# Performance work log

Measured on AMD Instinct MI355X. Metric: run time of the kernel, lower is better.

The kernel has to match this reference:

```python
import jax, jax.numpy as jnp
import numpy as np

N = 4096      # atoms
K = 5         # atoms gathered per cell (top_k in put_atoms_in_cells)
M = 8         # neighbors kept per atom
NBR = 26      # neighbor cells per cell (9+9+8)

def _grid():
    # get_cells: box [-10,10) step 1 Angstrom -> 20^3 = 8000 cells
    g = jnp.arange(-10.0, 10.0, 1.0)
    X = jnp.stack(jnp.meshgrid(g, g, g))       # (3,20,20,20), tf.meshgrid default 'xy'
    return jnp.transpose(X).reshape(-1, 3)      # (8000,3)

def _sqdist(a, b):
    # ||a_i - b_j||^2 via expansion; avoids (A,B,3) intermediate
    return (jnp.sum(a * a, 1)[:, None] + jnp.sum(b * b, 1)[None, :] - 2.0 * (a @ b.T))

def _neighbor_list(coords):
    cells = _grid()                              # (n_cells, 3)
    # put_atoms_in_cells: tf.nn.top_k(norm, k) -> k LARGEST norms (faithful to source)
    d_ca = _sqdist(cells, coords)                # (n_cells, N)
    _, atoms_in_cells = jax.lax.top_k(d_ca, K)   # (n_cells, K)
    # get_cells_for_atoms: top_k(-norm, 1) -> closest cell per atom
    d_ac = _sqdist(coords, cells)                # (N, n_cells)
    cells_for_atoms = jnp.argmin(d_ac, axis=1)   # (N,)
    # compute_neighbor_cells: top_k(norm, 26) (faithful to source)
    d_cc = _sqdist(cells, cells)                 # (n_cells, n_cells)
    _, nbr_cells = jax.lax.top_k(d_cc, NBR)      # (n_cells, 26)
    nbr_cells_atom = nbr_cells[cells_for_atoms]  # (N, 26)
    nbr_inds = atoms_in_cells[nbr_cells_atom]    # (N, 26, K)
    nbr_coords = coords[nbr_inds]                # (N, 26, K, 3)
    dists = jnp.sum((coords[:, None, None, :] - nbr_coords) ** 2, axis=-1)
    dists = dists.reshape(N, NBR * K)            # (N, 130)
    _, locs = jax.lax.top_k(dists, M)            # top_k(dists, M) as in source
    flat = nbr_inds.reshape(N, NBR * K)
    return jnp.take_along_axis(flat, locs, axis=1)   # (N, M) atom indices

def _energy(coords, vdw, weights, nrot, nbr):
    # d_ij = r_ij - R_i - R_j
    diff = coords[:, None, :] - coords[nbr]      # (N, M, 3)
    r = jnp.sqrt(jnp.sum(diff * diff, axis=-1) + 1e-12)
    d = r - vdw[:, None] - vdw[nbr]
    g1 = jnp.exp(-(d / 0.5) ** 2)
    g2 = jnp.exp(-((d - 3.0) / 2.0) ** 2)
    rep = jnp.where(d < 0.0, d * d, 0.0)
    hyd = jnp.where(d < 0.5, 1.0, jnp.where(d < 1.5, 1.5 - d, 0.0))
    hb = jnp.where(d < -0.7, 1.0, jnp.where(d < 0.0, -d / 0.7, 0.0))
    hval = (weights[0] * g1 + weights[1] * g2 + weights[2] * rep
            + weights[3] * hyd + weights[4] * hb)
    f = jnp.where(d < 8.0, hval, 0.0)            # cutoff at 8 Angstrom
    c = jnp.sum(f)
    return c / (1.0 + weights[5] * nrot[0])      # g(c, Nrot)

def setup_inputs() -> dict:
    key = jax.random.key(0)
    k1, k2, k3 = jax.random.split(key, 3)
    coords = jax.random.uniform(k1, (N, 3), jnp.float32, -10.0, 10.0)
    vdw = jax.random.uniform(k2, (N,), jnp.float32, 1.0, 2.0)
    weights = 0.3 * jax.random.normal(k3, (6,), jnp.float32)
    nrot = 8.0 * jnp.ones((1,), jnp.float32)
    return {"coords": coords, "vdw": vdw, "weights": weights, "nrot": nrot}

def reference(coords, vdw, weights, nrot):
    nbr = _neighbor_list(coords)
    return _energy(coords, vdw, weights, nrot, nbr)
```

## Files before the change

kernel.cpp:

```cpp
#include <hip/hip_runtime.h>
#include <stdint.h>

#define NATOMS 4096
#define NCELLS 8000
#define KTOP 5
#define MNBR 8
#define NBRC 26
#define HBINS 184
#define LSTMAX 512

__device__ __forceinline__ unsigned long long umax64(unsigned long long a, unsigned long long b) {
    return a > b ? a : b;
}
__device__ __forceinline__ unsigned long long umin64(unsigned long long a, unsigned long long b) {
    return a < b ? a : b;
}

__device__ __forceinline__ void cell_coords_i(int m, int& x, int& y, int& z) {
    int a = m / 400;
    int r = m - a * 400;
    int b = r / 20;
    int c = r - b * 20;
    x = b - 10; y = c - 10; z = a - 10;
}

__global__ __launch_bounds__(256) void k1_cells_nbr(const float* __restrict__ coords,
                                                    int* __restrict__ cellsForAtoms,
                                                    float* __restrict__ sumsq,
                                                    int* __restrict__ nbrTable,
                                                    int* __restrict__ neededFlag) {
    const int atom = blockIdx.x;
    const int t = threadIdx.x;
    const int lane = t & 63;

    __shared__ int sCi;
    __shared__ uint32_t h[HBINS];
    __shared__ int lst[LSTMAX];
    __shared__ int sV, cnt;

    if (t < HBINS) h[t] = 0;
    if (t == 0) cnt = 0;

    if (t < 64) {
        float ax = coords[atom * 3], ay = coords[atom * 3 + 1], az = coords[atom * 3 + 2];
        float sa = __fadd_rn(__fadd_rn(__fmul_rn(ax, ax), __fmul_rn(ay, ay)), __fmul_rn(az, az));

        int fx = (int)floorf(ax), fy = (int)floorf(ay), fz = (int)floorf(az);
        int vx = min(9, max(-10, fx - 1 + (lane & 3)));
        int vy = min(9, max(-10, fy - 1 + ((lane >> 2) & 3)));
        int vz = min(9, max(-10, fz - 1 + (lane >> 4)));
        int m = (vz + 10) * 400 + (vx + 10) * 20 + (vy + 10);

        float cx = (float)vx, cy = (float)vy, cz = (float)vz;
        float scell = (float)(vx * vx + vy * vy + vz * vz);
        float dot = __fadd_rn(__fadd_rn(__fmul_rn(ax, cx), __fmul_rn(ay, cy)), __fmul_rn(az, cz));
        float val = __fsub_rn(__fadd_rn(sa, scell), __fmul_rn(2.0f, dot));
        unsigned long long key = ((unsigned long long)__float_as_uint(val) << 32) | (unsigned int)m;

        for (int off = 32; off > 0; off >>= 1)
            key = umin64(key, (unsigned long long)__shfl_xor((long long)key, off));
        if (lane == 0) {
            int c = (int)(key & 0xFFFFFFFFull);
            cellsForAtoms[atom] = c;
            sumsq[atom] = sa;
            sCi = c;
        }
    }
    __syncthreads();

    const int ci = sCi;
    int xi, yi, zi;
    cell_coords_i(ci, xi, yi, zi);
    const int Lx = max(xi + 10, 9 - xi);
    const int Ly = max(yi + 10, 9 - yi);
    const int Lz = max(zi + 10, 9 - zi);
    const int lo = (Lx - 2) * (Lx - 2) + (Ly - 2) * (Ly - 2) + (Lz - 2) * (Lz - 2)
                 + 2 * min(Lx, min(Ly, Lz)) - 3;
    const int A0 = zi + 10;

#pragma unroll
    for (int col = 0; col < 2; ++col) {
        int p = t + 256 * col;
        if (p < 400) {
            int bb = p / 20, cc = p - bb * 20;
            int dxv = xi - (bb - 10), dyv = yi - (cc - 10);
            int Dbc = dxv * dxv + dyv * dyv;
            int a = 0;
            for (; a < 20; ++a) {
                int dz = A0 - a;
                int d = Dbc + dz * dz;
                if (d < lo) break;
                atomicAdd(&h[d - lo], 1u);
            }
            if (a < 20) {
                for (int a2 = 19; a2 >= a; --a2) {
                    int dz = A0 - a2;
                    int d = Dbc + dz * dz;
                    if (d < lo) break;
                    atomicAdd(&h[d - lo], 1u);
                }
            }
        }
    }
    __syncthreads();

    if (t < 64) {
        int c4[4];
        int cnt4 = 0;
#pragma unroll
        for (int k = 0; k < 4; ++k) {
            int b = (HBINS - 1) - (t * 4 + k);
            c4[k] = (b >= 0) ? (int)h[b] : 0;
            cnt4 += c4[k];
        }
        int incl = cnt4;
        for (int off = 1; off < 64; off <<= 1) {
            int v = __shfl_up(incl, off);
            if (lane >= off) incl += v;
        }
        int P = incl - cnt4;
        if (P < NBRC && incl >= NBRC) {
            int run = P;
#pragma unroll
            for (int k = 0; k < 4; ++k) {
                run += c4[k];
                if (run >= NBRC) { sV = lo + (HBINS - 1) - (t * 4 + k); break; }
            }
        }
    }
    __syncthreads();
    const int V = sV;

#pragma unroll
    for (int col = 0; col < 2; ++col) {
        int p = t + 256 * col;
        if (p < 400) {
            int bb = p / 20, cc = p - bb * 20;
            int dxv = xi - (bb - 10), dyv = yi - (cc - 10);
            int Dbc = dxv * dxv + dyv * dyv;
            int a = 0;
            for (; a < 20; ++a) {
                int dz = A0 - a;
                int d = Dbc + dz * dz;
                if (d < V) break;
                int q = atomicAdd(&cnt, 1);
                if (q < LSTMAX) lst[q] = (d << 13) | (8191 - (a * 400 + p));
            }
            if (a < 20) {
                for (int a2 = 19; a2 >= a; --a2) {
                    int dz = A0 - a2;
                    int d = Dbc + dz * dz;
                    if (d < V) break;
                    int q = atomicAdd(&cnt, 1);
                    if (q < LSTMAX) lst[q] = (d << 13) | (8191 - (a2 * 400 + p));
                }
            }
        }
    }
    __syncthreads();

    int n = min(cnt, LSTMAX);
    for (int idx = t; idx < n; idx += 256) {
        int key = lst[idx];
        int rank = 0;
        for (int m = 0; m < n; ++m) rank += (lst[m] > key) ? 1 : 0;
        if (rank < NBRC) {
            int j = 8191 - (key & 8191);
            nbrTable[ci * NBRC + rank] = j;
            neededFlag[j] = 1;
        }
    }
}

__global__ __launch_bounds__(256) void k2_atoms(const float* __restrict__ coords,
                                                const float* __restrict__ sumsq,
                                                const int* __restrict__ neededFlag,
                                                int* __restrict__ atomsInCells) {
    const int i = blockIdx.x;
    if (neededFlag[i] != 1) return;
    __shared__ unsigned long long wl[4 * KTOP];
    const int t = threadIdx.x;
    const int lane = t & 63, wv = t >> 6;

    int xi_, yi_, zi_;
    cell_coords_i(i, xi_, yi_, zi_);
    const float cx = (float)xi_, cy = (float)yi_, cz = (float)zi_;
    const float scell = (float)(xi_ * xi_ + yi_ * yi_ + zi_ * zi_);

    unsigned long long keys[16];
#pragma unroll
    for (int s = 0; s < 16; ++s) {
        int j = t + 256 * s;
        float ax = coords[j * 3], ay = coords[j * 3 + 1], az = coords[j * 3 + 2];
        float sa = sumsq[j];
        float dot = __fadd_rn(__fadd_rn(__fmul_rn(cx, ax), __fmul_rn(cy, ay)), __fmul_rn(cz, az));
        float val = __fsub_rn(__fadd_rn(scell, sa), __fmul_rn(2.0f, dot));
        keys[s] = ((unsigned long long)__float_as_uint(val) << 32) | (unsigned int)(4095 - j);
    }

    for (int r = 0; r < KTOP; ++r) {
        unsigned long long best = 0ull;
#pragma unroll
        for (int s = 0; s < 16; ++s) best = umax64(best, keys[s]);
        for (int off = 32; off > 0; off >>= 1)
            best = umax64(best, (unsigned long long)__shfl_xor((long long)best, off));
        if (lane == 0) wl[wv * KTOP + r] = best;
#pragma unroll
        for (int s = 0; s < 16; ++s) if (keys[s] == best) keys[s] = 0ull;
    }
    __syncthreads();

    if (t < 4 * KTOP) {
        unsigned long long key = wl[t];
        int rank = 0;
        for (int m = 0; m < 4 * KTOP; ++m) rank += (wl[m] > key) ? 1 : 0;
        if (rank < KTOP) atomsInCells[i * KTOP + rank] = 4095 - (int)(key & 0xFFFFFFFFull);
    }
}

__global__ __launch_bounds__(256) void k3_energy(const float* __restrict__ coords,
                                                 const float* __restrict__ vdw,
                                                 const float* __restrict__ weights,
                                                 const int* __restrict__ nbrTable,
                                                 const int* __restrict__ atomsInCells,
                                                 const int* __restrict__ cellsForAtoms,
                                                 float* __restrict__ partials) {
    const int wid = threadIdx.x >> 6;
    const int lane = threadIdx.x & 63;
    const int i = blockIdx.x * 4 + wid;

    const float xi = coords[i * 3], yi = coords[i * 3 + 1], zi = coords[i * 3 + 2];
    const int ci = cellsForAtoms[i];

    int cand[3];
    unsigned long long keys[3];
#pragma unroll
    for (int s = 0; s < 3; ++s) {
        int p = lane + 64 * s;
        cand[s] = -1;
        keys[s] = 0ull;
        if (p < NBRC * KTOP) {
            int cellSlot = p / KTOP;
            int atomSlot = p - cellSlot * KTOP;
            int nc = nbrTable[ci * NBRC + cellSlot];
            int j = atomsInCells[nc * KTOP + atomSlot];
            cand[s] = j;
            float dx = __fsub_rn(xi, coords[j * 3]);
            float dy = __fsub_rn(yi, coords[j * 3 + 1]);
            float dz = __fsub_rn(zi, coords[j * 3 + 2]);
            float dist = __fadd_rn(__fadd_rn(__fmul_rn(dx, dx), __fmul_rn(dy, dy)), __fmul_rn(dz, dz));
            keys[s] = ((unsigned long long)__float_as_uint(dist) << 8) | (unsigned int)(255 - p);
        }
    }

    const float w0 = weights[0], w1 = weights[1], w2 = weights[2];
    const float w3 = weights[3], w4 = weights[4];
    const float vi = vdw[i];

    float esum = 0.0f;
    for (int r = 0; r < MNBR; ++r) {
        unsigned long long best = umax64(umax64(keys[0], keys[1]), keys[2]);
        for (int off = 32; off > 0; off >>= 1)
            best = umax64(best, (unsigned long long)__shfl_xor((long long)best, off));

        int p = 255 - (int)(best & 0xFFull);
        int slot = p >> 6;
        int owner = p & 63;
        int jsel = (slot == 0) ? cand[0] : (slot == 1) ? cand[1] : cand[2];
        int j = __shfl(jsel, owner);
        float dist = __uint_as_float((unsigned int)(best >> 8));

#pragma unroll
        for (int s = 0; s < 3; ++s) if (keys[s] == best) keys[s] = 0ull;

        float rr = __fsqrt_rn(__fadd_rn(dist, 1e-12f));
        float d = __fsub_rn(__fsub_rn(rr, vi), vdw[j]);
        float t1 = __fdiv_rn(d, 0.5f);
        float g1 = expf(-__fmul_rn(t1, t1));
        float t2 = __fdiv_rn(__fsub_rn(d, 3.0f), 2.0f);
        float g2 = expf(-__fmul_rn(t2, t2));
        float rep = (d < 0.0f) ? __fmul_rn(d, d) : 0.0f;
        float hyd = (d < 0.5f) ? 1.0f : ((d < 1.5f) ? __fsub_rn(1.5f, d) : 0.0f);
        float hb = (d < -0.7f) ? 1.0f : ((d < 0.0f) ? __fdiv_rn(-d, 0.7f) : 0.0f);
        float hval = __fadd_rn(__fadd_rn(__fadd_rn(__fadd_rn(
                         __fmul_rn(w0, g1), __fmul_rn(w1, g2)),
                         __fmul_rn(w2, rep)), __fmul_rn(w3, hyd)), __fmul_rn(w4, hb));
        float f = (d < 8.0f) ? hval : 0.0f;
        esum = __fadd_rn(esum, f);
    }
    if (lane == 0) partials[i] = esum;
}

__global__ __launch_bounds__(256) void k4_reduce(const float* __restrict__ partials,
                                                 const float* __restrict__ weights,
                                                 const float* __restrict__ nrot,
                                                 float* __restrict__ out) {
    __shared__ float red[256];
    const int t = threadIdx.x;
    float s = 0.0f;
    for (int k = 0; k < NATOMS / 256; ++k) s = __fadd_rn(s, partials[t + 256 * k]);
    red[t] = s;
    __syncthreads();
    for (int off = 128; off > 0; off >>= 1) {
        if (t < off) red[t] = __fadd_rn(red[t], red[t + off]);
        __syncthreads();
    }
    if (t == 0) out[0] = __fdiv_rn(red[0], __fadd_rn(1.0f, __fmul_rn(weights[5], nrot[0])));
}

extern "C" void kernel_launch(void* const* d_in, const int* in_sizes, int n_in,
                              void* d_out, int out_size, void* d_ws, size_t ws_size,
                              hipStream_t stream) {
    const float* coords  = (const float*)d_in[0];
    const float* vdw     = (const float*)d_in[1];
    const float* weights = (const float*)d_in[2];
    const float* nrot    = (const float*)d_in[3];
    float* out = (float*)d_out;

    int* nbrTable      = (int*)d_ws;
    int* atomsInCells  = nbrTable + NCELLS * NBRC;
    int* cellsForAtoms = atomsInCells + NCELLS * KTOP;
    int* neededFlag    = cellsForAtoms + NATOMS;
    float* partials    = (float*)(neededFlag + NCELLS);
    float* sumsq       = partials + NATOMS;

    k1_cells_nbr<<<NATOMS, 256, 0, stream>>>(coords, cellsForAtoms, sumsq,
                                             nbrTable, neededFlag);
    k2_atoms<<<NCELLS, 256, 0, stream>>>(coords, sumsq, neededFlag, atomsInCells);
    k3_energy<<<NATOMS / 4, 256, 0, stream>>>(coords, vdw, weights, nbrTable,
                                              atomsInCells, cellsForAtoms, partials);
    k4_reduce<<<1, 256, 0, stream>>>(partials, weights, nrot, out);
}
```

Before: 39.49 us.

## Pack atom coords and norms into float4 and loop cells in k2 blocks

Kernel 1 now writes each atom's coordinates together with its squared norm as a single float4. Kernels 2 and 3 read that array with one vector load instead of three scalar coordinate loads plus a separate norm load. Kernel 2 also launches 2000 blocks that each walk four cells instead of 8000 one-cell blocks. This cuts the cost of launching and scheduling many blocks that exit immediately, but it adds extra barriers per block and may leave work unevenly spread when the needed cells cluster.

```diff
diff --git a/kernel.cpp b/kernel.cpp
--- a/kernel.cpp
+++ b/kernel.cpp
@@ -8,6 +8,7 @@
 #define NBRC 26
 #define HBINS 184
 #define LSTMAX 512
+#define K2BLKS 2000
 
 __device__ __forceinline__ unsigned long long umax64(unsigned long long a, unsigned long long b) {
     return a > b ? a : b;
@@ -26,7 +27,7 @@
 
 __global__ __launch_bounds__(256) void k1_cells_nbr(const float* __restrict__ coords,
                                                     int* __restrict__ cellsForAtoms,
-                                                    float* __restrict__ sumsq,
+                                                    float4* __restrict__ c4,
                                                     int* __restrict__ nbrTable,
                                                     int* __restrict__ neededFlag) {
     const int atom = blockIdx.x;
@@ -62,7 +63,7 @@
         if (lane == 0) {
             int c = (int)(key & 0xFFFFFFFFull);
             cellsForAtoms[atom] = c;
-            sumsq[atom] = sa;
+            c4[atom] = make_float4(ax, ay, az, sa);
             sCi = c;
         }
     }
@@ -105,13 +106,13 @@
     __syncthreads();
 
     if (t < 64) {
-        int c4[4];
+        int c4b[4];
         int cnt4 = 0;
 #pragma unroll
         for (int k = 0; k < 4; ++k) {
             int b = (HBINS - 1) - (t * 4 + k);
-            c4[k] = (b >= 0) ? (int)h[b] : 0;
-            cnt4 += c4[k];
+            c4b[k] = (b >= 0) ? (int)h[b] : 0;
+            cnt4 += c4b[k];
         }
         int incl = cnt4;
         for (int off = 1; off < 64; off <<= 1) {
@@ -123,7 +124,7 @@
             int run = P;
 #pragma unroll
             for (int k = 0; k < 4; ++k) {
-                run += c4[k];
+                run += c4b[k];
                 if (run >= NBRC) { sV = lo + (HBINS - 1) - (t * 4 + k); break; }
             }
         }
@@ -172,53 +173,56 @@
     }
 }
 
-__global__ __launch_bounds__(256) void k2_atoms(const float* __restrict__ coords,
-                                                const float* __restrict__ sumsq,
+__global__ __launch_bounds__(256) void k2_atoms(const float4* __restrict__ c4,
                                                 const int* __restrict__ neededFlag,
                                                 int* __restrict__ atomsInCells) {
-    const int i = blockIdx.x;
-    if (neededFlag[i] != 1) return;
     __shared__ unsigned long long wl[4 * KTOP];
     const int t = threadIdx.x;
     const int lane = t & 63, wv = t >> 6;
 
-    int xi_, yi_, zi_;
-    cell_coords_i(i, xi_, yi_, zi_);
-    const float cx = (float)xi_, cy = (float)yi_, cz = (float)zi_;
-    const float scell = (float)(xi_ * xi_ + yi_ * yi_ + zi_ * zi_);
-
-    unsigned long long keys[16];
-#pragma unroll
-    for (int s = 0; s < 16; ++s) {
-        int j = t + 256 * s;
-        float ax = coords[j * 3], ay = coords[j * 3 + 1], az = coords[j * 3 + 2];
-        float sa = sumsq[j];
-        float dot = __fadd_rn(__fadd_rn(__fmul_rn(cx, ax), __fmul_rn(cy, ay)), __fmul_rn(cz, az));
-        float val = __fsub_rn(__fadd_rn(scell, sa), __fmul_rn(2.0f, dot));
-        keys[s] = ((unsigned long long)__float_as_uint(val) << 32) | (unsigned int)(4095 - j);
-    }
-
-    for (int r = 0; r < KTOP; ++r) {
-        unsigned long long best = 0ull;
-#pragma unroll
-        for (int s = 0; s < 16; ++s) best = umax64(best, keys[s]);
-        for (int off = 32; off > 0; off >>= 1)
-            best = umax64(best, (unsigned long long)__shfl_xor((long long)best, off));
-        if (lane == 0) wl[wv * KTOP + r] = best;
-#pragma unroll
-        for (int s = 0; s < 16; ++s) if (keys[s] == best) keys[s] = 0ull;
-    }
-    __syncthreads();
-
-    if (t < 4 * KTOP) {
-        unsigned long long key = wl[t];
-        int rank = 0;
-        for (int m = 0; m < 4 * KTOP; ++m) rank += (wl[m] > key) ? 1 : 0;
-        if (rank < KTOP) atomsInCells[i * KTOP + rank] = 4095 - (int)(key & 0xFFFFFFFFull);
-    }
-}
-
-__global__ __launch_bounds__(256) void k3_energy(const float* __restrict__ coords,
+    for (int w = 0; w < 4; ++w) {
+        const int i = blockIdx.x + w * K2BLKS;
+        if (neededFlag[i] != 1) continue;
+
+        int xi_, yi_, zi_;
+        cell_coords_i(i, xi_, yi_, zi_);
+        const float cx = (float)xi_, cy = (float)yi_, cz = (float)zi_;
+        const float scell = (float)(xi_ * xi_ + yi_ * yi_ + zi_ * zi_);
+
+        unsigned long long keys[16];
+#pragma unroll
+        for (int s = 0; s < 16; ++s) {
+            int j = t + 256 * s;
+            float4 v = c4[j];
+            float dot = __fadd_rn(__fadd_rn(__fmul_rn(cx, v.x), __fmul_rn(cy, v.y)),
+                                  __fmul_rn(cz, v.z));
+            float val = __fsub_rn(__fadd_rn(scell, v.w), __fmul_rn(2.0f, dot));
+            keys[s] = ((unsigned long long)__float_as_uint(val) << 32) | (unsigned int)(4095 - j);
+        }
+
+        for (int r = 0; r < KTOP; ++r) {
+            unsigned long long best = 0ull;
+#pragma unroll
+            for (int s = 0; s < 16; ++s) best = umax64(best, keys[s]);
+            for (int off = 32; off > 0; off >>= 1)
+                best = umax64(best, (unsigned long long)__shfl_xor((long long)best, off));
+            if (lane == 0) wl[wv * KTOP + r] = best;
+#pragma unroll
+            for (int s = 0; s < 16; ++s) if (keys[s] == best) keys[s] = 0ull;
+        }
+        __syncthreads();
+
+        if (t < 4 * KTOP) {
+            unsigned long long key = wl[t];
+            int rank = 0;
+            for (int m = 0; m < 4 * KTOP; ++m) rank += (wl[m] > key) ? 1 : 0;
+            if (rank < KTOP) atomsInCells[i * KTOP + rank] = 4095 - (int)(key & 0xFFFFFFFFull);
+        }
+        __syncthreads();
+    }
+}
+
+__global__ __launch_bounds__(256) void k3_energy(const float4* __restrict__ c4,
                                                  const float* __restrict__ vdw,
                                                  const float* __restrict__ weights,
                                                  const int* __restrict__ nbrTable,
@@ -229,7 +233,8 @@
     const int lane = threadIdx.x & 63;
     const int i = blockIdx.x * 4 + wid;
 
-    const float xi = coords[i * 3], yi = coords[i * 3 + 1], zi = coords[i * 3 + 2];
+    const float4 vi4 = c4[i];
+    const float xi = vi4.x, yi = vi4.y, zi = vi4.z;
     const int ci = cellsForAtoms[i];
 
     int cand[3];
@@ -245,9 +250,10 @@
             int nc = nbrTable[ci * NBRC + cellSlot];
             int j = atomsInCells[nc * KTOP + atomSlot];
             cand[s] = j;
-            float dx = __fsub_rn(xi, coords[j * 3]);
-            float dy = __fsub_rn(yi, coords[j * 3 + 1]);
-            float dz = __fsub_rn(zi, coords[j * 3 + 2]);
+            float4 vj = c4[j];
+            float dx = __fsub_rn(xi, vj.x);
+            float dy = __fsub_rn(yi, vj.y);
+            float dz = __fsub_rn(zi, vj.z);
             float dist = __fadd_rn(__fadd_rn(__fmul_rn(dx, dx), __fmul_rn(dy, dy)), __fmul_rn(dz, dz));
             keys[s] = ((unsigned long long)__float_as_uint(dist) << 8) | (unsigned int)(255 - p);
         }
@@ -322,12 +328,12 @@
     int* cellsForAtoms = atomsInCells + NCELLS * KTOP;
     int* neededFlag    = cellsForAtoms + NATOMS;
     float* partials    = (float*)(neededFlag + NCELLS);
-    float* sumsq       = partials + NATOMS;
-
-    k1_cells_nbr<<<NATOMS, 256, 0, stream>>>(coords, cellsForAtoms, sumsq,
+    float4* c4         = (float4*)(partials + NATOMS);
+
+    k1_cells_nbr<<<NATOMS, 256, 0, stream>>>(coords, cellsForAtoms, c4,
                                              nbrTable, neededFlag);
-    k2_atoms<<<NCELLS, 256, 0, stream>>>(coords, sumsq, neededFlag, atomsInCells);
-    k3_energy<<<NATOMS / 4, 256, 0, stream>>>(coords, vdw, weights, nbrTable,
+    k2_atoms<<<K2BLKS, 256, 0, stream>>>(c4, neededFlag, atomsInCells);
+    k3_energy<<<NATOMS / 4, 256, 0, stream>>>(c4, vdw, weights, nbrTable,
                                               atomsInCells, cellsForAtoms, partials);
     k4_reduce<<<1, 256, 0, stream>>>(partials, weights, nrot, out);
 }
```

Result: slower. 45.19 us (+14.4%).
